# Kernel tuning notes

Measured on AMD Instinct MI355X. Metric: run time of the kernel, lower is better.

The kernel has to match this reference:

```python
import jax, jax.numpy as jnp
import numpy as np

B, D, T, K = 16, 512, 4096, 1024
COMMIT = 0.25


def setup_inputs() -> dict:
    key = jax.random.key(0)
    kx, ke = jax.random.split(key)
    x = jax.random.normal(kx, (B, D, T), dtype=jnp.float32)
    # nn.init.uniform_(weight, -1/K, 1/K)
    embedding = jax.random.uniform(ke, (K, D), dtype=jnp.float32,
                                   minval=-1.0 / K, maxval=1.0 / K)
    return {"x": x, "embedding": embedding}


def reference(x, embedding):
    # x: [B, D, T] -> [B, T, D]
    xt = jnp.transpose(x, (0, 2, 1))
    xf = xt.reshape(-1, xt.shape[-1])  # [N, D], N = B*T
    dist = (jnp.sum(xf * xf, axis=1, keepdims=True)
            + jnp.sum(embedding * embedding, axis=1)
            - 2.0 * (xf @ embedding.T))
    idx = jnp.argmin(dist, axis=1)  # [N]
    # one-hot @ embedding == gather
    quantized = jnp.take(embedding, idx, axis=0).reshape(xt.shape)  # [B, T, D]
    commitment_loss = COMMIT * jnp.mean((jax.lax.stop_gradient(quantized) - xt) ** 2)
    embedding_loss = jnp.mean((quantized - jax.lax.stop_gradient(xt)) ** 2)
    loss = commitment_loss + embedding_loss
    # straight-through estimator
    quantized_st = xt + jax.lax.stop_gradient(quantized - xt)
    encoding_indices = idx.reshape(xt.shape[0], xt.shape[1], 1)
    return quantized_st, loss, encoding_indices
```

## Files before the change

### kernel.cpp

```cpp
#include <hip/hip_runtime.h>

#define BB 16
#define DD 512
#define TT 4096
#define KK 1024
#define NN (BB*TT)
#define RWS 32
#define BT 512
#define NW 8
#define MARGIN 1e-3f
#define CM 6
#define XLD 516
#define NPART (NN/RWS)

typedef __attribute__((ext_vector_type(8))) short short8v;
typedef __attribute__((ext_vector_type(4))) float f32x4;

__device__ __forceinline__ unsigned short f2bf(float f) {
    unsigned int u = __float_as_uint(f);
    unsigned int r = (u + 0x7fffu + ((u >> 16) & 1u)) >> 16;
    return (unsigned short)r;
}

__device__ __forceinline__ unsigned int f2sort(float f) {
    unsigned int b = __float_as_uint(f);
    return (b & 0x80000000u) ? ~b : (b | 0x80000000u);
}
__device__ __forceinline__ float sort2f(unsigned int u) {
    unsigned int b = (u & 0x80000000u) ? (u & 0x7fffffffu) : ~u;
    return __uint_as_float(b);
}

__device__ __forceinline__ float pw128_sq_strided(const float* a, int stride) {
    float V[16];
    #pragma unroll
    for (int l = 0; l < 16; ++l) {
        float q[8];
        #pragma unroll
        for (int k = 0; k < 8; ++k) {
            float e = a[(l + 16 * k) * stride];
            q[k] = __fmul_rn(e, e);
        }
        V[l] = __fadd_rn(__fadd_rn(__fadd_rn(q[0], q[1]), __fadd_rn(q[2], q[3])),
                         __fadd_rn(__fadd_rn(q[4], q[5]), __fadd_rn(q[6], q[7])));
    }
    float u[8];
    #pragma unroll
    for (int l = 0; l < 8; ++l) u[l] = __fadd_rn(V[l], V[l + 8]);
    float v[4];
    #pragma unroll
    for (int l = 0; l < 4; ++l) v[l] = __fadd_rn(u[l], u[l + 4]);
    return __fadd_rn(__fadd_rn(v[0], v[2]), __fadd_rn(v[1], v[3]));
}
__device__ __forceinline__ float pw512_sq_strided(const float* a, int stride) {
    float p0 = pw128_sq_strided(a, stride);
    float p1 = pw128_sq_strided(a + 128 * stride, stride);
    float p2 = pw128_sq_strided(a + 256 * stride, stride);
    float p3 = pw128_sq_strided(a + 384 * stride, stride);
    return __fadd_rn(__fadd_rn(p0, p1), __fadd_rn(p2, p3));
}

__global__ void enorms_exact(const float* __restrict__ E, float* __restrict__ se) {
    int i = blockIdx.x * blockDim.x + threadIdx.x;
    if (i < KK) se[i] = pw512_sq_strided(E + (long)i * DD, 1);
}

__global__ void pack_e(const float* __restrict__ E, unsigned short* __restrict__ Bph) {
    int i = blockIdx.x * blockDim.x + threadIdx.x;
    if (i >= KK * DD / 2) return;
    int c = i >> 8;
    int k = (i & 255) * 2;
    float2 v = *reinterpret_cast<const float2*>(E + ((long)c << 9) + k);
    int lane = (c & 15) + ((k >> 3) & 3) * 16;
    int hw = (((c >> 4) * 16 + (k >> 5)) * 64 + lane) * 8 + (k & 7);
    unsigned int pk = (unsigned int)f2bf(v.x) | ((unsigned int)f2bf(v.y) << 16);
    *reinterpret_cast<unsigned int*>(Bph + hw) = pk;
}

__device__ __forceinline__ short8v build_frag_rm(const float* __restrict__ row, int c0) {
    union { short8v v; unsigned int wd[4]; } u;
    float4 a = *reinterpret_cast<const float4*>(row + c0);
    float4 b = *reinterpret_cast<const float4*>(row + c0 + 4);
    asm("v_cvt_pk_bf16_f32 %0, %1, %2" : "=v"(u.wd[0]) : "v"(a.x), "v"(a.y));
    asm("v_cvt_pk_bf16_f32 %0, %1, %2" : "=v"(u.wd[1]) : "v"(a.z), "v"(a.w));
    asm("v_cvt_pk_bf16_f32 %0, %1, %2" : "=v"(u.wd[2]) : "v"(b.x), "v"(b.y));
    asm("v_cvt_pk_bf16_f32 %0, %1, %2" : "=v"(u.wd[3]) : "v"(b.z), "v"(b.w));
    return u.v;
}

__global__ __launch_bounds__(BT)
void vq_fused(const float* __restrict__ x, const float* __restrict__ E,
              const unsigned short* __restrict__ Bph,
              const float* __restrict__ se,
              double* __restrict__ partials, float* __restrict__ out) {
    __shared__ __align__(16) float xsf[RWS * XLD];
    __shared__ unsigned int rowmin[RWS];
    __shared__ int   rcnt[RWS];
    __shared__ unsigned short rc[RWS][CM];
    __shared__ unsigned long long rmin[RWS];
    __shared__ float sxs[RWS];
    __shared__ int   fidx[RWS];
    __shared__ int   oflag[RWS];
    __shared__ double wloss[NW];
    __shared__ int   oany;

    const int tid  = threadIdx.x;
    const int w    = tid >> 6;
    const int lane = tid & 63;
    const int blk  = blockIdx.x;
    const int b    = blk >> 7;
    const int t0   = (blk & 127) * RWS;
    const long nbase = (long)b * TT + t0;
    const float* xb = x + (long)b * DD * TT + t0;

    if (tid < RWS) {
        rcnt[tid] = 0; rowmin[tid] = 0xFFFFFFFFu; rmin[tid] = ~0ull;
        oflag[tid] = 0; fidx[tid] = -1;
    }
    if (tid == 0) oany = 0;

    {
        const int r  = lane & 31;
        const int dh = lane >> 5;
        const float* xbl = xb + r;
        #pragma unroll
        for (int it = 0; it < 4; ++it) {
            int d0 = ((it * NW + w) * 2 + dh) * 8;
            float v[8];
            #pragma unroll
            for (int jj = 0; jj < 8; ++jj)
                v[jj] = xbl[(long)(d0 + jj) * TT];
            float4 lo = {v[0], v[1], v[2], v[3]};
            float4 hi = {v[4], v[5], v[6], v[7]};
            *reinterpret_cast<float4*>(&xsf[r * XLD + d0])     = lo;
            *reinterpret_cast<float4*>(&xsf[r * XLD + d0 + 4]) = hi;
        }
    }
    __syncthreads();

    f32x4 acc[2][8];
    #pragma unroll
    for (int m = 0; m < 2; ++m)
        #pragma unroll
        for (int n = 0; n < 8; ++n)
            acc[m][n] = (f32x4){0.f, 0.f, 0.f, 0.f};

    const short8v* Bhv = (const short8v*)Bph;
    {
        const int rl  = lane & 15;
        const int lg8 = (lane >> 4) * 8;
        for (int kk = 0; kk < 16; ++kk) {
            short8v ah[2];
            #pragma unroll
            for (int m = 0; m < 2; ++m)
                ah[m] = build_frag_rm(xsf + (m * 16 + rl) * XLD, kk * 32 + lg8);
            #pragma unroll
            for (int nh = 0; nh < 2; ++nh) {
                short8v bh[4];
                #pragma unroll
                for (int q = 0; q < 4; ++q)
                    bh[q] = Bhv[((w * 8 + nh * 4 + q) * 16 + kk) * 64 + lane];
                __builtin_amdgcn_s_setprio(1);
                #pragma unroll
                for (int q = 0; q < 4; ++q)
                    #pragma unroll
                    for (int m = 0; m < 2; ++m)
                        acc[m][nh * 4 + q] = __builtin_amdgcn_mfma_f32_16x16x32_bf16(
                            ah[m], bh[q], acc[m][nh * 4 + q], 0, 0, 0);
                __builtin_amdgcn_s_setprio(0);
            }
        }
    }

    float sef[8];
    #pragma unroll
    for (int n = 0; n < 8; ++n) sef[n] = se[w * 128 + n * 16 + (lane & 15)];

    #pragma unroll
    for (int m = 0; m < 2; ++m) {
        #pragma unroll
        for (int r4 = 0; r4 < 4; ++r4) {
            float mn = 1e30f;
            #pragma unroll
            for (int n = 0; n < 8; ++n)
                mn = fminf(mn, fmaf(-2.f, acc[m][n][r4], sef[n]));
            #pragma unroll
            for (int off = 1; off < 16; off <<= 1)
                mn = fminf(mn, __shfl_xor(mn, off, 64));
            if ((lane & 15) == 0)
                atomicMin(&rowmin[m * 16 + (lane >> 4) * 4 + r4], f2sort(mn));
        }
    }
    {
        int r = tid >> 4, l = tid & 15;
        const float* bp = xsf + r * XLD;
        float pblk[4];
        #pragma unroll
        for (int kb = 0; kb < 4; ++kb) {
            float q[8];
            #pragma unroll
            for (int k = 0; k < 8; ++k) {
                float e = bp[kb * 128 + l + 16 * k];
                q[k] = __fmul_rn(e, e);
            }
            float V = __fadd_rn(__fadd_rn(__fadd_rn(q[0], q[1]), __fadd_rn(q[2], q[3])),
                                __fadd_rn(__fadd_rn(q[4], q[5]), __fadd_rn(q[6], q[7])));
            V = __fadd_rn(V, __shfl_xor(V, 8, 16));
            V = __fadd_rn(V, __shfl_xor(V, 4, 16));
            V = __fadd_rn(V, __shfl_xor(V, 2, 16));
            V = __fadd_rn(V, __shfl_xor(V, 1, 16));
            pblk[kb] = V;
        }
        if (l == 0)
            sxs[r] = __fadd_rn(__fadd_rn(pblk[0], pblk[1]), __fadd_rn(pblk[2], pblk[3]));
    }
    __syncthreads();

    #pragma unroll
    for (int m = 0; m < 2; ++m) {
        #pragma unroll
        for (int r4 = 0; r4 < 4; ++r4) {
            int row = m * 16 + (lane >> 4) * 4 + r4;
            float th = sort2f(rowmin[row]) + MARGIN;
            #pragma unroll
            for (int n = 0; n < 8; ++n) {
                float sc = fmaf(-2.f, acc[m][n][r4], sef[n]);
                if (sc <= th) {
                    int pos = atomicAdd(&rcnt[row], 1);
                    if (pos < CM)
                        rc[row][pos] = (unsigned short)(w * 128 + n * 16 + (lane & 15));
                }
            }
        }
    }
    __syncthreads();

    if (lane < 24) {
        int s = lane * 8 + w;
        int r = s / CM, ci = s - r * CM;
        int cnt = rcnt[r];
        if (cnt >= 2 && cnt <= CM && ci < cnt) {
            int c = (int)rc[r][ci];
            const float4* Ep4 = reinterpret_cast<const float4*>(E + (long)c * DD);
            const float4* Xp4 = reinterpret_cast<const float4*>(xsf + r * XLD);
            float g = 0.f;
            #pragma unroll 4
            for (int jj = 0; jj < 128; ++jj) {
                float4 e4 = Ep4[jj], x4 = Xp4[jj];
                g = __fmaf_rn(x4.x, e4.x, g);
                g = __fmaf_rn(x4.y, e4.y, g);
                g = __fmaf_rn(x4.z, e4.z, g);
                g = __fmaf_rn(x4.w, e4.w, g);
            }
            float t1 = __fadd_rn(sxs[r], se[c]);
            float d  = __fsub_rn(t1, __fmul_rn(2.f, g));
            unsigned long long key = ((unsigned long long)f2sort(d) << 10) | (unsigned int)c;
            atomicMin(&rmin[r], key);
        }
    }
    __syncthreads();

    if (tid < RWS) {
        int cnt = rcnt[tid];
        if (cnt == 1)                   fidx[tid] = (int)rc[tid][0];
        else if (cnt >= 2 && cnt <= CM) fidx[tid] = (int)(rmin[tid] & 0x3ffu);
        else { oflag[tid] = 1; atomicOr(&oany, 1); }
    }
    __syncthreads();

    if (oany) {
        for (int r = 0; r < RWS; ++r) {
            if (!oflag[r]) continue;
            const float4* Xp4 = reinterpret_cast<const float4*>(xsf + r * XLD);
            float bd = 1e30f; int bi = KK;
            #pragma unroll
            for (int q = 0; q < 2; ++q) {
                int c = q * BT + tid;
                const float4* Ep4 = reinterpret_cast<const float4*>(E + (long)c * DD);
                float g = 0.f;
                #pragma unroll 4
                for (int jj = 0; jj < 128; ++jj) {
                    float4 e4 = Ep4[jj], x4 = Xp4[jj];
                    g = __fmaf_rn(x4.x, e4.x, g);
                    g = __fmaf_rn(x4.y, e4.y, g);
                    g = __fmaf_rn(x4.z, e4.z, g);
                    g = __fmaf_rn(x4.w, e4.w, g);
                }
                float d = __fsub_rn(__fadd_rn(sxs[r], se[c]), __fmul_rn(2.f, g));
                if (d < bd) { bd = d; bi = c; }
            }
            #pragma unroll
            for (int off = 32; off; off >>= 1) {
                float tv = __shfl_down(bd, off, 64);
                int   ti = __shfl_down(bi, off, 64);
                if (tv < bd || (tv == bd && ti < bi)) { bd = tv; bi = ti; }
            }
            if (lane == 0) {
                unsigned long long key = ((unsigned long long)f2sort(bd) << 10) | (unsigned int)bi;
                atomicMin(&rmin[r], key);
            }
            __syncthreads();
            if (tid == 0) fidx[r] = (int)(rmin[r] & 0x3ffu);
            __syncthreads();
        }
        __syncthreads();
    }

    if (tid < RWS)
        out[(size_t)NN * DD + 1 + nbase + tid] = (float)fidx[tid];

    float lacc = 0.f;
    #pragma unroll
    for (int it = 0; it < 8; ++it) {
        int flat = it * BT + tid;
        int r = flat >> 7;
        int j = (flat & 127) * 4;
        int idx = fidx[r];
        float4 ev = *reinterpret_cast<const float4*>(E + (long)idx * DD + j);
        float4 xv = *reinterpret_cast<const float4*>(&xsf[r * XLD + j]);
        float d0 = __fsub_rn(ev.x, xv.x);
        float d1 = __fsub_rn(ev.y, xv.y);
        float d2 = __fsub_rn(ev.z, xv.z);
        float d3 = __fsub_rn(ev.w, xv.w);
        float4 st;
        st.x = __fadd_rn(xv.x, d0); st.y = __fadd_rn(xv.y, d1);
        st.z = __fadd_rn(xv.z, d2); st.w = __fadd_rn(xv.w, d3);
        *reinterpret_cast<float4*>(out + (size_t)(nbase + r) * DD + j) = st;
        lacc = __fmaf_rn(d0, d0, lacc);
        lacc = __fmaf_rn(d1, d1, lacc);
        lacc = __fmaf_rn(d2, d2, lacc);
        lacc = __fmaf_rn(d3, d3, lacc);
    }
    double dl = (double)lacc;
    #pragma unroll
    for (int off = 32; off; off >>= 1) dl += __shfl_down(dl, off, 64);
    if (lane == 0) wloss[w] = dl;
    __syncthreads();
    if (tid == 0) {
        double s = 0.0;
        #pragma unroll
        for (int ww = 0; ww < NW; ++ww) s += wloss[ww];
        partials[blk] = s;
    }
}

__global__ void finalize_kernel(const double* __restrict__ partials, float* __restrict__ out) {
    __shared__ double sm[16];
    const int tid = threadIdx.x;
    const int w = tid >> 6, lane = tid & 63;
    double a = partials[tid] + partials[tid + 1024];
    #pragma unroll
    for (int off = 32; off; off >>= 1) a += __shfl_down(a, off, 64);
    if (lane == 0) sm[w] = a;
    __syncthreads();
    if (tid == 0) {
        double s = 0.0;
        #pragma unroll
        for (int i = 0; i < 16; ++i) s += sm[i];
        out[(size_t)NN * DD] = (float)(1.25 * s / ((double)NN * DD));
    }
}

extern "C" void kernel_launch(void* const* d_in, const int* in_sizes, int n_in,
                              void* d_out, int out_size, void* d_ws, size_t ws_size,
                              hipStream_t stream) {
    const float* x = (const float*)d_in[0];
    const float* E = (const float*)d_in[1];
    float* out = (float*)d_out;
    double* partials = (double*)d_ws;
    float* se = (float*)((char*)d_ws + 32768);
    unsigned short* Bph = (unsigned short*)((char*)d_ws + 65536);

    enorms_exact<<<4, 256, 0, stream>>>(E, se);
    pack_e<<<(KK * DD / 2) / 256, 256, 0, stream>>>(E, Bph);
    vq_fused<<<NPART, BT, 0, stream>>>(x, E, Bph, se, partials, out);
    finalize_kernel<<<1, 1024, 0, stream>>>(partials, out);
}
```

Measured before the change: 207.7 us.

## Switch distance GEMM from bf16 MFMA to int8 MFMA with per-row scales

Quantizes x rows and codebook rows to int8 using per-row absmax scales and computes the candidate-screening dot products with i32 16x16x64 int8 MFMA, halving the K-loop iterations and B-operand bytes. Dequantized scores feed the same rowmin/margin candidate selection, with margin and candidate cap widened to cover the larger quantization error, and candidates are still re-scored exactly in fp32. It adds a per-row absmax reduction and risks more ambiguous rows falling through to the slower fallback path.

```diff
diff --git a/kernel.cpp b/kernel.cpp
--- a/kernel.cpp
+++ b/kernel.cpp
@@ -8,19 +8,13 @@
 #define RWS 32
 #define BT 512
 #define NW 8
-#define MARGIN 1e-3f
-#define CM 6
+#define MARGIN 2e-3f
+#define CM 8
 #define XLD 516
 #define NPART (NN/RWS)
-
-typedef __attribute__((ext_vector_type(8))) short short8v;
-typedef __attribute__((ext_vector_type(4))) float f32x4;
-
-__device__ __forceinline__ unsigned short f2bf(float f) {
-    unsigned int u = __float_as_uint(f);
-    unsigned int r = (u + 0x7fffu + ((u >> 16) & 1u)) >> 16;
-    return (unsigned short)r;
-}
+#define INV127 0.007874015748f
+
+typedef __attribute__((ext_vector_type(4))) int int4v;
 
 __device__ __forceinline__ unsigned int f2sort(float f) {
     unsigned int b = __float_as_uint(f);
@@ -29,6 +23,15 @@
 __device__ __forceinline__ float sort2f(unsigned int u) {
     unsigned int b = (u & 0x80000000u) ? (u & 0x7fffffffu) : ~u;
     return __uint_as_float(b);
+}
+
+__device__ __forceinline__ unsigned int q4(float4 v, float inv) {
+    const float MG = 12582912.0f;
+    unsigned int b0 = __float_as_uint(__fmaf_rn(v.x, inv, MG));
+    unsigned int b1 = __float_as_uint(__fmaf_rn(v.y, inv, MG));
+    unsigned int b2 = __float_as_uint(__fmaf_rn(v.z, inv, MG));
+    unsigned int b3 = __float_as_uint(__fmaf_rn(v.w, inv, MG));
+    return (b0 & 0xFFu) | ((b1 & 0xFFu) << 8) | ((b2 & 0xFFu) << 16) | (b3 << 24);
 }
 
 __device__ __forceinline__ float pw128_sq_strided(const float* a, int stride) {
@@ -60,40 +63,47 @@
     return __fadd_rn(__fadd_rn(p0, p1), __fadd_rn(p2, p3));
 }
 
-__global__ void enorms_exact(const float* __restrict__ E, float* __restrict__ se) {
+__global__ void enorms_exact(const float* __restrict__ E, float* __restrict__ se,
+                             float* __restrict__ sesc) {
     int i = blockIdx.x * blockDim.x + threadIdx.x;
-    if (i < KK) se[i] = pw512_sq_strided(E + (long)i * DD, 1);
-}
-
-__global__ void pack_e(const float* __restrict__ E, unsigned short* __restrict__ Bph) {
+    if (i >= KK) return;
+    const float* Ep = E + (long)i * DD;
+    se[i] = pw512_sq_strided(Ep, 1);
+    float am = 0.f;
+    for (int j = 0; j < DD; ++j) am = fmaxf(am, fabsf(Ep[j]));
+    sesc[i] = am * INV127;
+}
+
+__global__ void pack_e_i8(const float* __restrict__ E, const float* __restrict__ sesc,
+                          unsigned int* __restrict__ Bq) {
     int i = blockIdx.x * blockDim.x + threadIdx.x;
-    if (i >= KK * DD / 2) return;
-    int c = i >> 8;
-    int k = (i & 255) * 2;
-    float2 v = *reinterpret_cast<const float2*>(E + ((long)c << 9) + k);
-    int lane = (c & 15) + ((k >> 3) & 3) * 16;
-    int hw = (((c >> 4) * 16 + (k >> 5)) * 64 + lane) * 8 + (k & 7);
-    unsigned int pk = (unsigned int)f2bf(v.x) | ((unsigned int)f2bf(v.y) << 16);
-    *reinterpret_cast<unsigned int*>(Bph + hw) = pk;
-}
-
-__device__ __forceinline__ short8v build_frag_rm(const float* __restrict__ row, int c0) {
-    union { short8v v; unsigned int wd[4]; } u;
-    float4 a = *reinterpret_cast<const float4*>(row + c0);
-    float4 b = *reinterpret_cast<const float4*>(row + c0 + 4);
-    asm("v_cvt_pk_bf16_f32 %0, %1, %2" : "=v"(u.wd[0]) : "v"(a.x), "v"(a.y));
-    asm("v_cvt_pk_bf16_f32 %0, %1, %2" : "=v"(u.wd[1]) : "v"(a.z), "v"(a.w));
-    asm("v_cvt_pk_bf16_f32 %0, %1, %2" : "=v"(u.wd[2]) : "v"(b.x), "v"(b.y));
-    asm("v_cvt_pk_bf16_f32 %0, %1, %2" : "=v"(u.wd[3]) : "v"(b.z), "v"(b.w));
-    return u.v;
+    if (i >= KK * DD / 4) return;
+    int c = i >> 7;
+    int k = (i & 127) * 4;
+    float inv = 1.0f / sesc[c];
+    float4 v = *reinterpret_cast<const float4*>(E + ((long)c << 9) + k);
+    int lane = (c & 15) + ((k >> 4) & 3) * 16;
+    int w32 = (((c >> 4) * 8 + (k >> 6)) * 64 + lane) * 4 + ((k & 15) >> 2);
+    Bq[w32] = q4(v, inv);
+}
+
+__device__ __forceinline__ int4v build_frag_i8(const float* __restrict__ row,
+                                               int c0, float inv) {
+    int4v r;
+    #pragma unroll
+    for (int q = 0; q < 4; ++q)
+        r[q] = (int)q4(*reinterpret_cast<const float4*>(row + c0 + q * 4), inv);
+    return r;
 }
 
 __global__ __launch_bounds__(BT)
 void vq_fused(const float* __restrict__ x, const float* __restrict__ E,
-              const unsigned short* __restrict__ Bph,
-              const float* __restrict__ se,
+              const unsigned int* __restrict__ Bq,
+              const float* __restrict__ se, const float* __restrict__ sesc,
               double* __restrict__ partials, float* __restrict__ out) {
     __shared__ __align__(16) float xsf[RWS * XLD];
+    __shared__ float pwmax[NW * RWS];
+    __shared__ float rowamax[RWS];
     __shared__ unsigned int rowmin[RWS];
     __shared__ int   rcnt[RWS];
     __shared__ unsigned short rc[RWS][CM];
@@ -123,73 +133,108 @@
         const int r  = lane & 31;
         const int dh = lane >> 5;
         const float* xbl = xb + r;
+        float am = 0.f;
         #pragma unroll
         for (int it = 0; it < 4; ++it) {
             int d0 = ((it * NW + w) * 2 + dh) * 8;
             float v[8];
             #pragma unroll
-            for (int jj = 0; jj < 8; ++jj)
+            for (int jj = 0; jj < 8; ++jj) {
                 v[jj] = xbl[(long)(d0 + jj) * TT];
+                am = fmaxf(am, fabsf(v[jj]));
+            }
             float4 lo = {v[0], v[1], v[2], v[3]};
             float4 hi = {v[4], v[5], v[6], v[7]};
             *reinterpret_cast<float4*>(&xsf[r * XLD + d0])     = lo;
             *reinterpret_cast<float4*>(&xsf[r * XLD + d0 + 4]) = hi;
         }
-    }
-    __syncthreads();
-
-    f32x4 acc[2][8];
+        am = fmaxf(am, __shfl_xor(am, 32, 64));
+        if (lane < 32) pwmax[w * RWS + r] = am;
+    }
+    __syncthreads();
+
+    if (tid < RWS) {
+        float rm = pwmax[tid];
+        #pragma unroll
+        for (int ww = 1; ww < NW; ++ww) rm = fmaxf(rm, pwmax[ww * RWS + tid]);
+        rowamax[tid] = rm;
+    }
+
+    int4v acc[2][8];
     #pragma unroll
     for (int m = 0; m < 2; ++m)
         #pragma unroll
         for (int n = 0; n < 8; ++n)
-            acc[m][n] = (f32x4){0.f, 0.f, 0.f, 0.f};
-
-    const short8v* Bhv = (const short8v*)Bph;
+            acc[m][n] = (int4v){0, 0, 0, 0};
+
+    const int rl   = lane & 15;
+    const int lg16 = (lane >> 4) * 16;
+    float rm0, rm1;
     {
-        const int rl  = lane & 15;
-        const int lg8 = (lane >> 4) * 8;
-        for (int kk = 0; kk < 16; ++kk) {
-            short8v ah[2];
-            #pragma unroll
-            for (int m = 0; m < 2; ++m)
-                ah[m] = build_frag_rm(xsf + (m * 16 + rl) * XLD, kk * 32 + lg8);
-            #pragma unroll
-            for (int nh = 0; nh < 2; ++nh) {
-                short8v bh[4];
+        float a0 = pwmax[rl], a1 = pwmax[16 + rl];
+        #pragma unroll
+        for (int ww = 1; ww < NW; ++ww) {
+            a0 = fmaxf(a0, pwmax[ww * RWS + rl]);
+            a1 = fmaxf(a1, pwmax[ww * RWS + 16 + rl]);
+        }
+        rm0 = a0; rm1 = a1;
+    }
+    const float inv0 = 127.0f / rm0;
+    const float inv1 = 127.0f / rm1;
+
+    const int4v* Bqv = (const int4v*)Bq;
+    for (int kk = 0; kk < 8; ++kk) {
+        int4v ah[2];
+        ah[0] = build_frag_i8(xsf + rl * XLD,        kk * 64 + lg16, inv0);
+        ah[1] = build_frag_i8(xsf + (16 + rl) * XLD, kk * 64 + lg16, inv1);
+        #pragma unroll
+        for (int nh = 0; nh < 2; ++nh) {
+            int4v bq[4];
+            #pragma unroll
+            for (int q = 0; q < 4; ++q)
+                bq[q] = Bqv[((w * 8 + nh * 4 + q) * 8 + kk) * 64 + lane];
+            __builtin_amdgcn_s_setprio(1);
+            #pragma unroll
+            for (int q = 0; q < 4; ++q)
                 #pragma unroll
-                for (int q = 0; q < 4; ++q)
-                    bh[q] = Bhv[((w * 8 + nh * 4 + q) * 16 + kk) * 64 + lane];
-                __builtin_amdgcn_s_setprio(1);
-                #pragma unroll
-                for (int q = 0; q < 4; ++q)
-                    #pragma unroll
-                    for (int m = 0; m < 2; ++m)
-                        acc[m][nh * 4 + q] = __builtin_amdgcn_mfma_f32_16x16x32_bf16(
-                            ah[m], bh[q], acc[m][nh * 4 + q], 0, 0, 0);
-                __builtin_amdgcn_s_setprio(0);
-            }
-        }
-    }
-
-    float sef[8];
-    #pragma unroll
-    for (int n = 0; n < 8; ++n) sef[n] = se[w * 128 + n * 16 + (lane & 15)];
+                for (int m = 0; m < 2; ++m)
+                    acc[m][nh * 4 + q] = __builtin_amdgcn_mfma_i32_16x16x64_i8(
+                        ah[m], bq[q], acc[m][nh * 4 + q], 0, 0, 0);
+            __builtin_amdgcn_s_setprio(0);
+        }
+    }
+
+    float sef[8], coef[8];
+    #pragma unroll
+    for (int n = 0; n < 8; ++n) {
+        int c = w * 128 + n * 16 + (lane & 15);
+        sef[n]  = se[c];
+        coef[n] = -2.0f * sesc[c];
+    }
 
     #pragma unroll
     for (int m = 0; m < 2; ++m) {
+        const float msx = __fmul_rn((m == 0) ? rm0 : rm1, INV127);
         #pragma unroll
         for (int r4 = 0; r4 < 4; ++r4) {
+            int row = m * 16 + (lane >> 4) * 4 + r4;
+            float rmr = pwmax[row];
+            #pragma unroll
+            for (int ww = 1; ww < NW; ++ww) rmr = fmaxf(rmr, pwmax[ww * RWS + row]);
+            float sxr = __fmul_rn(rmr, INV127);
             float mn = 1e30f;
             #pragma unroll
-            for (int n = 0; n < 8; ++n)
-                mn = fminf(mn, fmaf(-2.f, acc[m][n][r4], sef[n]));
+            for (int n = 0; n < 8; ++n) {
+                float d2 = __fmul_rn(sxr, coef[n]);
+                mn = fminf(mn, __fmaf_rn(d2, (float)acc[m][n][r4], sef[n]));
+            }
             #pragma unroll
             for (int off = 1; off < 16; off <<= 1)
                 mn = fminf(mn, __shfl_xor(mn, off, 64));
             if ((lane & 15) == 0)
-                atomicMin(&rowmin[m * 16 + (lane >> 4) * 4 + r4], f2sort(mn));
-        }
+                atomicMin(&rowmin[row], f2sort(mn));
+        }
+        (void)msx;
     }
     {
         int r = tid >> 4, l = tid & 15;
@@ -222,9 +267,11 @@
         for (int r4 = 0; r4 < 4; ++r4) {
             int row = m * 16 + (lane >> 4) * 4 + r4;
             float th = sort2f(rowmin[row]) + MARGIN;
+            float sxr = __fmul_rn(rowamax[row], INV127);
             #pragma unroll
             for (int n = 0; n < 8; ++n) {
-                float sc = fmaf(-2.f, acc[m][n][r4], sef[n]);
+                float d2 = __fmul_rn(sxr, coef[n]);
+                float sc = __fmaf_rn(d2, (float)acc[m][n][r4], sef[n]);
                 if (sc <= th) {
                     int pos = atomicAdd(&rcnt[row], 1);
                     if (pos < CM)
@@ -235,9 +282,8 @@
     }
     __syncthreads();
 
-    if (lane < 24) {
-        int s = lane * 8 + w;
-        int r = s / CM, ci = s - r * CM;
+    if (lane < 32) {
+        int r = lane, ci = w;
         int cnt = rcnt[r];
         if (cnt >= 2 && cnt <= CM && ci < cnt) {
             int c = (int)rc[r][ci];
@@ -368,11 +414,12 @@
     const float* E = (const float*)d_in[1];
     float* out = (float*)d_out;
     double* partials = (double*)d_ws;
-    float* se = (float*)((char*)d_ws + 32768);
-    unsigned short* Bph = (unsigned short*)((char*)d_ws + 65536);
-
-    enorms_exact<<<4, 256, 0, stream>>>(E, se);
-    pack_e<<<(KK * DD / 2) / 256, 256, 0, stream>>>(E, Bph);
-    vq_fused<<<NPART, BT, 0, stream>>>(x, E, Bph, se, partials, out);
+    float* se   = (float*)((char*)d_ws + 32768);
+    float* sesc = (float*)((char*)d_ws + 36864);
+    unsigned int* Bq = (unsigned int*)((char*)d_ws + 65536);
+
+    enorms_exact<<<4, 256, 0, stream>>>(E, se, sesc);
+    pack_e_i8<<<(KK * DD / 4) / 256, 256, 0, stream>>>(E, sesc, Bq);
+    vq_fused<<<NPART, BT, 0, stream>>>(x, E, Bq, se, sesc, partials, out);
     finalize_kernel<<<1, 1024, 0, stream>>>(partials, out);
 }
```

Result: slower. 267.8 us (+28.9%).
